# Kernel optimization log

Measured on AMD Instinct MI355X. Metric: run time of the kernel, lower is better.

Reference implementation:

```python
import jax, jax.numpy as jnp
import numpy as np

FEATURE_DIM = 2048
CROP_PE_DIM = 96
FULL = FEATURE_DIM + CROP_PE_DIM  # 2144
H1 = 1024
H2 = 512
NEG_SLOPE = 0.01


def leaky(x):
    return jnp.where(x >= 0, x, NEG_SLOPE * x)


def setup_inputs() -> dict:
    key = jax.random.key(0)
    ks = jax.random.split(key, 8)
    B, T = 512, 32
    features = jax.random.normal(ks[0], (B, T, FULL), dtype=jnp.float32)

    def lin(k, fan_in, fan_out):
        kw, kb = jax.random.split(k)
        bound = 1.0 / np.sqrt(fan_in)
        W = jax.random.uniform(kw, (fan_in, fan_out), minval=-bound, maxval=bound, dtype=jnp.float32)
        b = jax.random.uniform(kb, (fan_out,), minval=-bound, maxval=bound, dtype=jnp.float32)
        return W, b

    We, be = lin(ks[1], 2 * FULL, H1)
    W1a, b1a = lin(ks[2], H1, H1)
    W1b, b1b = lin(ks[3], H1, H2)
    W2a, b2a = lin(ks[4], H2, H2)
    W2b, b2b = lin(ks[5], H2, H2)
    Wd, bd = lin(ks[6], H2, 3)
    return {
        "features": features,
        "We": We, "be": be,
        "W1a": W1a, "b1a": b1a, "W1b": W1b, "b1b": b1b,
        "W2a": W2a, "b2a": b2a, "W2b": W2b, "b2b": b2b,
        "Wd": Wd, "bd": bd,
    }


def reference(features, We, be, W1a, b1a, W1b, b1b, W2a, b2a, W2b, b2b, Wd, bd):
    B, T, D = features.shape
    # Vectorized version of the double Python loop: pair each token with token 0.
    anchor = jnp.broadcast_to(features[:, :1, :], (B, T, D))  # features[i][0]
    features_full = jnp.concatenate((features, anchor), axis=-1).reshape(B * T, 2 * D)
    e_f = features_full @ We + be
    h = leaky(leaky(e_f) @ W1a + b1a)
    h = h @ W1b + b1b  # block1 output
    h2 = leaky(leaky(h) @ W2a + b2a) @ W2b + b2b  # block2
    h = h + h2
    translations = leaky(h) @ Wd + bd  # (B*T, 3)
    bias = jnp.array([[0.0, 0.0, 1.0]], dtype=translations.dtype)
    return translations + bias
```

## Files before the change

kernel.cpp:

```cpp
#include <hip/hip_runtime.h>
#include <hip/hip_bf16.h>
#include <stdint.h>

typedef __attribute__((ext_vector_type(4))) float f32x4;
typedef __attribute__((ext_vector_type(8))) short bf16x8;

#define BK 64

__device__ inline void gload_lds16(const void* g, void* l) {
    __builtin_amdgcn_global_load_lds(
        (const __attribute__((address_space(1))) void*)g,
        (__attribute__((address_space(3))) void*)l, 16, 0, 0);
}

__device__ inline void wg_barrier() {
    asm volatile("s_barrier" ::: "memory");
}
#define SCHED0 __builtin_amdgcn_sched_barrier(0)

__device__ inline int xcd_swizzle(int orig, int nwg) {
    int q = nwg >> 3, r = nwg & 7;
    int xcd = orig & 7, idx = orig >> 3;
    int base = (xcd < r) ? xcd * (q + 1) : r * (q + 1) + (xcd - r) * q;
    return base + idx;
}

__device__ inline float b2f(short s) {
    union { float f; unsigned u; } x; x.u = ((unsigned)(unsigned short)s) << 16; return x.f;
}
__device__ inline short f2bs(float f) {
    __hip_bfloat16 h = __float2bfloat16(f);
    short s; __builtin_memcpy(&s, &h, 2); return s;
}

__global__ __launch_bounds__(256) void cvt_feat(const float* __restrict__ in,
                                                __hip_bfloat16* __restrict__ out) {
    int i = blockIdx.x * 256 + threadIdx.x;
    const int CH = 16384 * 272;
    if (i >= CH) return;
    int r = i / 272, c8 = (i % 272) * 8;
    __hip_bfloat16 tmp[8];
    if (c8 < 2144) {
        const float4* p = (const float4*)(in + (size_t)r * 2144 + c8);
        float4 x0 = p[0], x1 = p[1];
        tmp[0] = __float2bfloat16(x0.x); tmp[1] = __float2bfloat16(x0.y);
        tmp[2] = __float2bfloat16(x0.z); tmp[3] = __float2bfloat16(x0.w);
        tmp[4] = __float2bfloat16(x1.x); tmp[5] = __float2bfloat16(x1.y);
        tmp[6] = __float2bfloat16(x1.z); tmp[7] = __float2bfloat16(x1.w);
    } else {
        #pragma unroll
        for (int j = 0; j < 8; j++) tmp[j] = __float2bfloat16(0.f);
    }
    *(bf16x8*)&out[(size_t)r * 2176 + c8] = *(const bf16x8*)tmp;
}

__global__ __launch_bounds__(256) void cvt_wt_t(const float* __restrict__ W,
                                                __hip_bfloat16* __restrict__ WT,
                                                int K, int N, int KP) {
    __shared__ float tile[32][33];
    const int ntn = N >> 5;
    const int tk = blockIdx.x / ntn, tn = blockIdx.x - tk * ntn;
    const int k0 = tk * 32, n0 = tn * 32;
    const int c = threadIdx.x & 31, r8 = threadIdx.x >> 5;
    #pragma unroll
    for (int p = 0; p < 4; p++) {
        int k = k0 + r8 + p * 8;
        tile[r8 + p * 8][c] = (k < K) ? W[(size_t)k * N + n0 + c] : 0.f;
    }
    __syncthreads();
    #pragma unroll
    for (int p = 0; p < 4; p++) {
        int n = n0 + r8 + p * 8;
        WT[(size_t)n * KP + k0 + c] = __float2bfloat16(tile[c][r8 + p * 8]);
    }
}

template<int BN_, int RES_MODE, int OUTK>
__global__ __launch_bounds__(512, 2)
void gemm8ph(const __hip_bfloat16* __restrict__ A, int lda,
             const __hip_bfloat16* __restrict__ Bt,
             const float* __restrict__ bias,
             const __hip_bfloat16* __restrict__ resb,
             const float* __restrict__ resf,
             __hip_bfloat16* __restrict__ outb,
             __hip_bfloat16* __restrict__ outb2,
             float* __restrict__ outf,
             int M, int N, int K, int gx)
{
    constexpr int NF  = BN_ / 64;
    constexpr int REL = NF * 16;
    __shared__ __hip_bfloat16 lds[2][(256 + BN_) * BK];

    const int nwg  = gridDim.x;
    const int wgid = xcd_swizzle(blockIdx.x, nwg);
    const int by   = wgid / gx;
    const int bx   = wgid - by * gx;

    const int t    = threadIdx.x;
    const int lane = t & 63;
    const int wv   = t >> 6;
    const int wr   = wv >> 2;
    const int wc   = wv & 3;

    const int row0 = by * 256;
    const int col0 = bx * BN_;

    const int NT = K / BK;
    const int split = blockIdx.y;
    const int kb = (split * NT) / gridDim.y;
    const int ke = ((split + 1) * NT) / gridDim.y;
    float* outfs = outf;
    if (OUTK == 0 && gridDim.y > 1) outfs = outf + (size_t)split * M * N;

    const int srow = t >> 3;
    const int scol = ((t & 7) * 8) ^ ((srow & 7) << 3);
    const int sdst = (t & 7) * 8;

    f32x4 acc[8][NF];
    #pragma unroll
    for (int i = 0; i < 8; i++)
        #pragma unroll
        for (int j = 0; j < NF; j++)
            acc[i][j] = f32x4{0.f, 0.f, 0.f, 0.f};

    const int lrow = lane & 15;
    const int lk   = (lane >> 4) * 8;
    const int rxor = (lrow & 7) << 3;

    auto stA = [&](int buf, int k0, int b) {
        gload_lds16(A + (size_t)(row0 + b * 64 + srow) * lda + k0 + scol,
                    &lds[buf][(b * 64 + srow) * BK + sdst]);
    };
    auto stB = [&](int buf, int k0, int b) {
        gload_lds16(Bt + (size_t)(col0 + b * 64 + srow) * K + k0 + scol,
                    &lds[buf][(256 + b * 64 + srow) * BK + sdst]);
    };
    auto rdA = [&](bf16x8 (&af)[4][2], int buf, int ih) {
        #pragma unroll
        for (int i = 0; i < 4; ++i)
            #pragma unroll
            for (int h = 0; h < 2; ++h)
                af[i][h] = *(const bf16x8*)
                    &lds[buf][(wr * 128 + (ih * 4 + i) * 16 + lrow) * BK + ((h * 32 + lk) ^ rxor)];
    };
    auto rdB = [&](bf16x8 (&bg)[2][2], int buf, int jb) {
        #pragma unroll
        for (int j = 0; j < 2; ++j)
            #pragma unroll
            for (int h = 0; h < 2; ++h)
                bg[j][h] = *(const bf16x8*)
                    &lds[buf][(256 + wc * REL + (jb + j) * 16 + lrow) * BK + ((h * 32 + lk) ^ rxor)];
    };

#define MFMA_Q(IB, JB)                                                        \
    do {                                                                      \
        __builtin_amdgcn_s_setprio(1);                                        \
        _Pragma("unroll") for (int h_ = 0; h_ < 2; ++h_)                      \
        _Pragma("unroll") for (int i_ = 0; i_ < 4; ++i_)                      \
        _Pragma("unroll") for (int j_ = 0; j_ < 2; ++j_)                      \
            acc[(IB) + i_][(JB) + j_] = __builtin_amdgcn_mfma_f32_16x16x32_bf16( \
                af[i_][h_], bg[j_][h_], acc[(IB) + i_][(JB) + j_], 0, 0, 0);  \
        __builtin_amdgcn_s_setprio(0);                                        \
    } while (0)

    {
        const int k0 = kb * BK;
        if constexpr (NF == 4) {
            stA(0, k0, 0); stA(0, k0, 2);
            stB(0, k0, 0); stB(0, k0, 1);
            stB(0, k0, 2); stB(0, k0, 3);
            stA(0, k0, 1); stA(0, k0, 3);
        } else {
            stA(0, k0, 0); stA(0, k0, 2);
            stB(0, k0, 0); stB(0, k0, 1);
            stA(0, k0, 1); stA(0, k0, 3);
        }
    }
    asm volatile("s_waitcnt vmcnt(2)" ::: "memory");
    wg_barrier();

    int cur = 0;
    for (int kt = kb; kt < ke; ++kt) {
        const bool pf = (kt + 1 < ke);
        const int nk0 = (kt + 1) * BK;
        bf16x8 af[4][2], bg[2][2];
        if constexpr (NF == 4) {
            rdA(af, cur, 0); rdB(bg, cur, 0);
            if (pf) { stA(cur ^ 1, nk0, 0); stA(cur ^ 1, nk0, 2); }
            wg_barrier(); SCHED0;
            MFMA_Q(0, 0);
            wg_barrier();
            rdB(bg, cur, 2);
            if (pf) { stB(cur ^ 1, nk0, 0); stB(cur ^ 1, nk0, 1); }
            if (pf) asm volatile("s_waitcnt vmcnt(4)" ::: "memory");
            else    asm volatile("s_waitcnt vmcnt(0)" ::: "memory");
            wg_barrier(); SCHED0;
            MFMA_Q(0, 2);
            wg_barrier();
            rdA(af, cur, 1); rdB(bg, cur, 0);
            if (pf) { stB(cur ^ 1, nk0, 2); stB(cur ^ 1, nk0, 3); }
            wg_barrier(); SCHED0;
            MFMA_Q(4, 0);
            wg_barrier();
            rdB(bg, cur, 2);
            if (pf) {
                stA(cur ^ 1, nk0, 1); stA(cur ^ 1, nk0, 3);
                asm volatile("s_waitcnt vmcnt(2)" ::: "memory");
            }
            wg_barrier(); SCHED0;
            MFMA_Q(4, 2);
            wg_barrier();
        } else {
            rdA(af, cur, 0); rdB(bg, cur, 0);
            if (pf) { stA(cur ^ 1, nk0, 0); stA(cur ^ 1, nk0, 2);
                      stB(cur ^ 1, nk0, 0); stB(cur ^ 1, nk0, 1); }
            if (pf) asm volatile("s_waitcnt vmcnt(4)" ::: "memory");
            else    asm volatile("s_waitcnt vmcnt(0)" ::: "memory");
            wg_barrier(); SCHED0;
            MFMA_Q(0, 0);
            wg_barrier();
            rdA(af, cur, 1);
            if (pf) {
                stA(cur ^ 1, nk0, 1); stA(cur ^ 1, nk0, 3);
                asm volatile("s_waitcnt vmcnt(2)" ::: "memory");
            }
            wg_barrier(); SCHED0;
            MFMA_Q(4, 0);
            wg_barrier();
        }
        cur ^= 1;
    }
#undef MFMA_Q

    if constexpr (OUTK == 0) {
        #pragma unroll
        for (int j = 0; j < NF; j++) {
            const int col = col0 + wc * REL + j * 16 + lrow;
            #pragma unroll
            for (int i = 0; i < 8; i++) {
                const int rbase = row0 + wr * 128 + i * 16 + (lane >> 4) * 4;
                #pragma unroll
                for (int r = 0; r < 4; r++)
                    outfs[(size_t)(rbase + r) * N + col] = acc[i][j][r];
            }
        }
    } else {
        wg_barrier();
        __hip_bfloat16* eb = &lds[0][0] + wv * (128 * REL);
        #pragma unroll
        for (int i = 0; i < 8; i++)
            #pragma unroll
            for (int j = 0; j < NF; j++)
                #pragma unroll
                for (int r = 0; r < 4; r++)
                    eb[(i * 16 + (lane >> 4) * 4 + r) * REL + j * 16 + lrow] =
                        __float2bfloat16(acc[i][j][r]);
        constexpr int LPR = REL / 8;
        constexpr int RPI = 64 / LPR;
        constexpr int NIT = 128 / RPI;
        const int lrr = lane / LPR;
        const int lcc = (lane % LPR) * 8;
        const int col = col0 + wc * REL + lcc;
        float bvv[8];
        if (bias) {
            float4 b0 = *(const float4*)&bias[col];
            float4 b1 = *(const float4*)&bias[col + 4];
            bvv[0] = b0.x; bvv[1] = b0.y; bvv[2] = b0.z; bvv[3] = b0.w;
            bvv[4] = b1.x; bvv[5] = b1.y; bvv[6] = b1.z; bvv[7] = b1.w;
        } else {
            #pragma unroll
            for (int e = 0; e < 8; e++) bvv[e] = 0.f;
        }
        #pragma unroll
        for (int it = 0; it < NIT; it++) {
            const int rl  = it * RPI + lrr;
            const int row = row0 + wr * 128 + rl;
            bf16x8 v8 = *(bf16x8*)&eb[rl * REL + lcc];
            float vv[8];
            #pragma unroll
            for (int e = 0; e < 8; e++) vv[e] = b2f(v8[e]) + bvv[e];
            if constexpr (RES_MODE == 1) {
                bf16x8 r8 = *(const bf16x8*)&resb[(size_t)row * N + col];
                #pragma unroll
                for (int e = 0; e < 8; e++) vv[e] += b2f(r8[e]);
            }
            if constexpr (RES_MODE == 2) {
                const float* rp = &resf[(size_t)(row >> 5) * N + col];
                float4 r0 = *(const float4*)rp;
                float4 r1 = *(const float4*)(rp + 4);
                vv[0] += r0.x; vv[1] += r0.y; vv[2] += r0.z; vv[3] += r0.w;
                vv[4] += r1.x; vv[5] += r1.y; vv[6] += r1.z; vv[7] += r1.w;
            }
            bf16x8 o1, o2;
            #pragma unroll
            for (int e = 0; e < 8; e++) {
                float lv = vv[e] >= 0.f ? vv[e] : 0.01f * vv[e];
                if constexpr (OUTK == 1) o1[e] = f2bs(lv);
                if constexpr (OUTK == 2) o1[e] = f2bs(vv[e]);
                if constexpr (OUTK == 3) { o1[e] = f2bs(lv); o2[e] = f2bs(vv[e]); }
            }
            *(bf16x8*)&outb[(size_t)row * N + col] = o1;
            if constexpr (OUTK == 3)
                *(bf16x8*)&outb2[(size_t)row * N + col] = o2;
        }
    }
}

__global__ __launch_bounds__(256)
void anchor_reduce(const float* __restrict__ part, const float* __restrict__ be,
                   float* __restrict__ out) {
    int i = blockIdx.x * 256 + threadIdx.x;
    if (i >= 512 * 1024) return;
    const int S = 512 * 1024;
    int col = i & 1023;
    float s = be[col];
    #pragma unroll
    for (int p = 0; p < 8; p++) s += part[i + p * S];
    out[i] = s;
}

__global__ __launch_bounds__(256)
void final_head(const __hip_bfloat16* __restrict__ h, const float* __restrict__ Wd,
                const float* __restrict__ bd, float* __restrict__ out)
{
    int row  = blockIdx.x * 4 + (threadIdx.x >> 6);
    int lane = threadIdx.x & 63;
    const __hip_bfloat16* hr = h + (size_t)row * 512;
    bf16x8 v8 = *(const bf16x8*)&hr[lane * 8];
    float s0 = 0.f, s1 = 0.f, s2 = 0.f;
    #pragma unroll
    for (int e = 0; e < 8; e++) {
        float v = b2f(v8[e]);
        v = v >= 0.f ? v : 0.01f * v;
        int k = lane * 8 + e;
        s0 += v * Wd[k * 3 + 0];
        s1 += v * Wd[k * 3 + 1];
        s2 += v * Wd[k * 3 + 2];
    }
    #pragma unroll
    for (int off = 32; off > 0; off >>= 1) {
        s0 += __shfl_down(s0, off);
        s1 += __shfl_down(s1, off);
        s2 += __shfl_down(s2, off);
    }
    if (lane == 0) {
        out[row * 3 + 0] = s0 + bd[0];
        out[row * 3 + 1] = s1 + bd[1];
        out[row * 3 + 2] = s2 + bd[2] + 1.0f;
    }
}

extern "C" void kernel_launch(void* const* d_in, const int* in_sizes, int n_in,
                              void* d_out, int out_size, void* d_ws, size_t ws_size,
                              hipStream_t stream)
{
    const float* features = (const float*)d_in[0];
    const float* We  = (const float*)d_in[1];
    const float* be  = (const float*)d_in[2];
    const float* W1a = (const float*)d_in[3];
    const float* b1a = (const float*)d_in[4];
    const float* W1b = (const float*)d_in[5];
    const float* b1b = (const float*)d_in[6];
    const float* W2a = (const float*)d_in[7];
    const float* b2a = (const float*)d_in[8];
    const float* W2b = (const float*)d_in[9];
    const float* b2b = (const float*)d_in[10];
    const float* Wd  = (const float*)d_in[11];
    const float* bd  = (const float*)d_in[12];
    float* out = (float*)d_out;

    char* ws = (char*)d_ws;
    size_t off = 0;
    auto alloc = [&](size_t bytes) -> char* {
        char* p = ws + off;
        off += (bytes + 255) & ~(size_t)255;
        return p;
    };
    __hip_bfloat16* featbf = (__hip_bfloat16*)alloc(16384ull * 2176 * 2);
    __hip_bfloat16* WeTt   = (__hip_bfloat16*)alloc(1024ull * 2176 * 2);
    __hip_bfloat16* WeTb   = (__hip_bfloat16*)alloc(1024ull * 2176 * 2);
    __hip_bfloat16* W1aT   = (__hip_bfloat16*)alloc(1024ull * 1024 * 2);
    __hip_bfloat16* W1bT   = (__hip_bfloat16*)alloc(512ull * 1024 * 2);
    __hip_bfloat16* W2aT   = (__hip_bfloat16*)alloc(512ull * 512 * 2);
    __hip_bfloat16* W2bT   = (__hip_bfloat16*)alloc(512ull * 512 * 2);
    float* eanchor_part    = (float*)alloc(8ull * 512 * 1024 * 4);
    float* eanchor         = (float*)alloc(512ull * 1024 * 4);
    char* bufA             = alloc(16384ull * 1024 * 2);
    char* bufB             = alloc(16384ull * 1024 * 2);
    __hip_bfloat16* h1b    = (__hip_bfloat16*)alloc(16384ull * 512 * 2);

    __hip_bfloat16* act1   = (__hip_bfloat16*)bufA;
    __hip_bfloat16* act2   = (__hip_bfloat16*)bufB;
    __hip_bfloat16* act3   = (__hip_bfloat16*)bufA;
    __hip_bfloat16* act4   = (__hip_bfloat16*)bufB;
    __hip_bfloat16* hsum_b = (__hip_bfloat16*)bufA;

    cvt_feat<<<(16384 * 272 + 255) / 256, 256, 0, stream>>>(features, featbf);
    cvt_wt_t<<<68 * 32, 256, 0, stream>>>(We,               WeTt, 2144, 1024, 2176);
    cvt_wt_t<<<68 * 32, 256, 0, stream>>>(We + 2144 * 1024, WeTb, 2144, 1024, 2176);
    cvt_wt_t<<<32 * 32, 256, 0, stream>>>(W1a, W1aT, 1024, 1024, 1024);
    cvt_wt_t<<<32 * 16, 256, 0, stream>>>(W1b, W1bT, 1024, 512, 1024);
    cvt_wt_t<<<16 * 16, 256, 0, stream>>>(W2a, W2aT, 512, 512, 512);
    cvt_wt_t<<<16 * 16, 256, 0, stream>>>(W2b, W2bT, 512, 512, 512);

    gemm8ph<256, 0, 0><<<dim3(8, 8), 512, 0, stream>>>(
        featbf, 32 * 2176, WeTb, nullptr, nullptr, nullptr,
        nullptr, nullptr, eanchor_part, 512, 1024, 2176, 4);
    anchor_reduce<<<2048, 256, 0, stream>>>(eanchor_part, be, eanchor);

    gemm8ph<256, 2, 1><<<dim3(256), 512, 0, stream>>>(
        featbf, 2176, WeTt, nullptr, nullptr, eanchor,
        act1, nullptr, nullptr, 16384, 1024, 2176, 4);

    gemm8ph<256, 0, 1><<<dim3(256), 512, 0, stream>>>(
        act1, 1024, W1aT, b1a, nullptr, nullptr,
        act2, nullptr, nullptr, 16384, 1024, 1024, 4);

    gemm8ph<128, 0, 3><<<dim3(256), 512, 0, stream>>>(
        act2, 1024, W1bT, b1b, nullptr, nullptr,
        act3, h1b, nullptr, 16384, 512, 1024, 4);

    gemm8ph<128, 0, 1><<<dim3(256), 512, 0, stream>>>(
        act3, 512, W2aT, b2a, nullptr, nullptr,
        act4, nullptr, nullptr, 16384, 512, 512, 4);

    gemm8ph<128, 1, 2><<<dim3(256), 512, 0, stream>>>(
        act4, 512, W2bT, b2b, h1b, nullptr,
        hsum_b, nullptr, nullptr, 16384, 512, 512, 4);

    final_head<<<4096, 256, 0, stream>>>(hsum_b, Wd, bd, out);
}
```

Baseline: 257.0 us.

## Fuse fp32-to-bf16 feature conversion into first GEMM's A-tile loads

Removes the separate cvt_feat kernel and its bf16 feature buffer. The encoder GEMMs now read fp32 features directly into registers, convert them to bf16, and write them into swizzled LDS, zero-padding the K tail. The main loop is also restructured to load all B fragments once per k-step and to issue A/B loads in consolidated groups with new waitcnt placement. This saves a full pass writing and re-reading 16384x2176 bf16, at the cost of doubling global A traffic (fp32) inside the GEMM and extra register pressure for the staging registers and B fragments.

```diff
diff --git a/kernel.cpp b/kernel.cpp
--- a/kernel.cpp
+++ b/kernel.cpp
@@ -31,27 +31,6 @@
 __device__ inline short f2bs(float f) {
     __hip_bfloat16 h = __float2bfloat16(f);
     short s; __builtin_memcpy(&s, &h, 2); return s;
-}
-
-__global__ __launch_bounds__(256) void cvt_feat(const float* __restrict__ in,
-                                                __hip_bfloat16* __restrict__ out) {
-    int i = blockIdx.x * 256 + threadIdx.x;
-    const int CH = 16384 * 272;
-    if (i >= CH) return;
-    int r = i / 272, c8 = (i % 272) * 8;
-    __hip_bfloat16 tmp[8];
-    if (c8 < 2144) {
-        const float4* p = (const float4*)(in + (size_t)r * 2144 + c8);
-        float4 x0 = p[0], x1 = p[1];
-        tmp[0] = __float2bfloat16(x0.x); tmp[1] = __float2bfloat16(x0.y);
-        tmp[2] = __float2bfloat16(x0.z); tmp[3] = __float2bfloat16(x0.w);
-        tmp[4] = __float2bfloat16(x1.x); tmp[5] = __float2bfloat16(x1.y);
-        tmp[6] = __float2bfloat16(x1.z); tmp[7] = __float2bfloat16(x1.w);
-    } else {
-        #pragma unroll
-        for (int j = 0; j < 8; j++) tmp[j] = __float2bfloat16(0.f);
-    }
-    *(bf16x8*)&out[(size_t)r * 2176 + c8] = *(const bf16x8*)tmp;
 }
 
 __global__ __launch_bounds__(256) void cvt_wt_t(const float* __restrict__ W,
@@ -75,21 +54,24 @@
     }
 }
 
-template<int BN_, int RES_MODE, int OUTK>
+template<int BN_, int RES_MODE, int OUTK, bool AF32>
 __global__ __launch_bounds__(512, 2)
-void gemm8ph(const __hip_bfloat16* __restrict__ A, int lda,
-             const __hip_bfloat16* __restrict__ Bt,
-             const float* __restrict__ bias,
-             const __hip_bfloat16* __restrict__ resb,
-             const float* __restrict__ resf,
-             __hip_bfloat16* __restrict__ outb,
-             __hip_bfloat16* __restrict__ outb2,
-             float* __restrict__ outf,
-             int M, int N, int K, int gx)
+void gemmk(const void* __restrict__ Asrc, int lda, int amult, int Kreal,
+           const __hip_bfloat16* __restrict__ Bt,
+           const float* __restrict__ bias,
+           const __hip_bfloat16* __restrict__ resb,
+           const float* __restrict__ resf,
+           __hip_bfloat16* __restrict__ outb,
+           __hip_bfloat16* __restrict__ outb2,
+           float* __restrict__ outf,
+           int M, int N, int K, int gx)
 {
     constexpr int NF  = BN_ / 64;
     constexpr int REL = NF * 16;
     __shared__ __hip_bfloat16 lds[2][(256 + BN_) * BK];
+
+    const float*          Af = (const float*)Asrc;
+    const __hip_bfloat16* Ab = (const __hip_bfloat16*)Asrc;
 
     const int nwg  = gridDim.x;
     const int wgid = xcd_swizzle(blockIdx.x, nwg);
@@ -113,8 +95,10 @@
     if (OUTK == 0 && gridDim.y > 1) outfs = outf + (size_t)split * M * N;
 
     const int srow = t >> 3;
-    const int scol = ((t & 7) * 8) ^ ((srow & 7) << 3);
-    const int sdst = (t & 7) * 8;
+    const int sc8  = (t & 7) * 8;
+    const int sswz = (srow & 7) << 3;
+    const int scol = sc8 ^ sswz;
+    const int sdst = sc8;
 
     f32x4 acc[8][NF];
     #pragma unroll
@@ -127,29 +111,58 @@
     const int lk   = (lane >> 4) * 8;
     const int rxor = (lrow & 7) << 3;
 
-    auto stA = [&](int buf, int k0, int b) {
-        gload_lds16(A + (size_t)(row0 + b * 64 + srow) * lda + k0 + scol,
-                    &lds[buf][(b * 64 + srow) * BK + sdst]);
-    };
-    auto stB = [&](int buf, int k0, int b) {
-        gload_lds16(Bt + (size_t)(col0 + b * 64 + srow) * K + k0 + scol,
-                    &lds[buf][(256 + b * 64 + srow) * BK + sdst]);
-    };
-    auto rdA = [&](bf16x8 (&af)[4][2], int buf, int ih) {
+    float4 sreg[8] = {};
+
+    auto stA_all = [&](int buf, int k0) {
+        #pragma unroll
+        for (int b = 0; b < 4; ++b)
+            gload_lds16(Ab + (size_t)(row0 + b * 64 + srow) * lda + k0 + scol,
+                        &lds[buf][(b * 64 + srow) * BK + sdst]);
+    };
+    auto ldA_all = [&](int k0) {
+        const int gc = k0 + sc8;
+        const bool v = gc < Kreal;
+        #pragma unroll
+        for (int b = 0; b < 4; ++b) {
+            const float* p = Af + (size_t)(row0 + b * 64 + srow) * (size_t)amult * lda + gc;
+            sreg[b * 2 + 0] = v ? *(const float4*)p       : float4{0.f, 0.f, 0.f, 0.f};
+            sreg[b * 2 + 1] = v ? *(const float4*)(p + 4) : float4{0.f, 0.f, 0.f, 0.f};
+        }
+    };
+    auto wrA_all = [&](int buf) {
+        #pragma unroll
+        for (int b = 0; b < 4; ++b) {
+            float4 x0 = sreg[b * 2], x1 = sreg[b * 2 + 1];
+            bf16x8 w;
+            w[0] = f2bs(x0.x); w[1] = f2bs(x0.y); w[2] = f2bs(x0.z); w[3] = f2bs(x0.w);
+            w[4] = f2bs(x1.x); w[5] = f2bs(x1.y); w[6] = f2bs(x1.z); w[7] = f2bs(x1.w);
+            *(bf16x8*)&lds[buf][(b * 64 + srow) * BK + (sc8 ^ sswz)] = w;
+        }
+    };
+    auto stB_all = [&](int buf, int k0) {
+        #pragma unroll
+        for (int b = 0; b < NF; ++b)
+            gload_lds16(Bt + (size_t)(col0 + b * 64 + srow) * K + k0 + scol,
+                        &lds[buf][(256 + b * 64 + srow) * BK + sdst]);
+    };
+
+    bf16x8 bgall[NF][2];
+    auto rdB_all = [&](int buf) {
+        #pragma unroll
+        for (int j = 0; j < NF; ++j)
+            #pragma unroll
+            for (int h = 0; h < 2; ++h)
+                bgall[j][h] = *(const bf16x8*)
+                    &lds[buf][(256 + wc * REL + j * 16 + lrow) * BK + ((h * 32 + lk) ^ rxor)];
+    };
+    bf16x8 af[4][2];
+    auto rdA = [&](int buf, int ih) {
         #pragma unroll
         for (int i = 0; i < 4; ++i)
             #pragma unroll
             for (int h = 0; h < 2; ++h)
                 af[i][h] = *(const bf16x8*)
                     &lds[buf][(wr * 128 + (ih * 4 + i) * 16 + lrow) * BK + ((h * 32 + lk) ^ rxor)];
-    };
-    auto rdB = [&](bf16x8 (&bg)[2][2], int buf, int jb) {
-        #pragma unroll
-        for (int j = 0; j < 2; ++j)
-            #pragma unroll
-            for (int h = 0; h < 2; ++h)
-                bg[j][h] = *(const bf16x8*)
-                    &lds[buf][(256 + wc * REL + (jb + j) * 16 + lrow) * BK + ((h * 32 + lk) ^ rxor)];
     };
 
 #define MFMA_Q(IB, JB)                                                        \
@@ -159,73 +172,75 @@
         _Pragma("unroll") for (int i_ = 0; i_ < 4; ++i_)                      \
         _Pragma("unroll") for (int j_ = 0; j_ < 2; ++j_)                      \
             acc[(IB) + i_][(JB) + j_] = __builtin_amdgcn_mfma_f32_16x16x32_bf16( \
-                af[i_][h_], bg[j_][h_], acc[(IB) + i_][(JB) + j_], 0, 0, 0);  \
+                af[i_][h_], bgall[(JB) + j_][h_], acc[(IB) + i_][(JB) + j_], 0, 0, 0); \
         __builtin_amdgcn_s_setprio(0);                                        \
     } while (0)
 
     {
         const int k0 = kb * BK;
-        if constexpr (NF == 4) {
-            stA(0, k0, 0); stA(0, k0, 2);
-            stB(0, k0, 0); stB(0, k0, 1);
-            stB(0, k0, 2); stB(0, k0, 3);
-            stA(0, k0, 1); stA(0, k0, 3);
+        if constexpr (AF32) {
+            ldA_all(k0);
+            stB_all(0, k0);
+            if constexpr (NF == 4) asm volatile("s_waitcnt vmcnt(4)" ::: "memory");
+            else                   asm volatile("s_waitcnt vmcnt(2)" ::: "memory");
+            wrA_all(0);
+            asm volatile("s_waitcnt vmcnt(0) lgkmcnt(0)" ::: "memory");
         } else {
-            stA(0, k0, 0); stA(0, k0, 2);
-            stB(0, k0, 0); stB(0, k0, 1);
-            stA(0, k0, 1); stA(0, k0, 3);
-        }
-    }
-    asm volatile("s_waitcnt vmcnt(2)" ::: "memory");
-    wg_barrier();
+            stA_all(0, k0);
+            stB_all(0, k0);
+            asm volatile("s_waitcnt vmcnt(0)" ::: "memory");
+        }
+        wg_barrier();
+    }
 
     int cur = 0;
     for (int kt = kb; kt < ke; ++kt) {
         const bool pf = (kt + 1 < ke);
         const int nk0 = (kt + 1) * BK;
-        bf16x8 af[4][2], bg[2][2];
         if constexpr (NF == 4) {
-            rdA(af, cur, 0); rdB(bg, cur, 0);
-            if (pf) { stA(cur ^ 1, nk0, 0); stA(cur ^ 1, nk0, 2); }
+            rdB_all(cur); rdA(cur, 0);
+            if (pf) { if constexpr (AF32) ldA_all(nk0); else stA_all(cur ^ 1, nk0); }
             wg_barrier(); SCHED0;
             MFMA_Q(0, 0);
             wg_barrier();
-            rdB(bg, cur, 2);
-            if (pf) { stB(cur ^ 1, nk0, 0); stB(cur ^ 1, nk0, 1); }
-            if (pf) asm volatile("s_waitcnt vmcnt(4)" ::: "memory");
-            else    asm volatile("s_waitcnt vmcnt(0)" ::: "memory");
+            if (pf) stB_all(cur ^ 1, nk0);
             wg_barrier(); SCHED0;
             MFMA_Q(0, 2);
             wg_barrier();
-            rdA(af, cur, 1); rdB(bg, cur, 0);
-            if (pf) { stB(cur ^ 1, nk0, 2); stB(cur ^ 1, nk0, 3); }
+            rdA(cur, 1);
+            if constexpr (AF32) {
+                if (pf) {
+                    asm volatile("s_waitcnt vmcnt(4)" ::: "memory");
+                    wrA_all(cur ^ 1);
+                }
+            }
             wg_barrier(); SCHED0;
             MFMA_Q(4, 0);
             wg_barrier();
-            rdB(bg, cur, 2);
+            MFMA_Q(4, 2);
+            if constexpr (AF32) asm volatile("s_waitcnt vmcnt(0) lgkmcnt(0)" ::: "memory");
+            else                asm volatile("s_waitcnt vmcnt(0)" ::: "memory");
+            wg_barrier();
+        } else {
+            rdB_all(cur); rdA(cur, 0);
             if (pf) {
-                stA(cur ^ 1, nk0, 1); stA(cur ^ 1, nk0, 3);
-                asm volatile("s_waitcnt vmcnt(2)" ::: "memory");
-            }
-            wg_barrier(); SCHED0;
-            MFMA_Q(4, 2);
-            wg_barrier();
-        } else {
-            rdA(af, cur, 0); rdB(bg, cur, 0);
-            if (pf) { stA(cur ^ 1, nk0, 0); stA(cur ^ 1, nk0, 2);
-                      stB(cur ^ 1, nk0, 0); stB(cur ^ 1, nk0, 1); }
-            if (pf) asm volatile("s_waitcnt vmcnt(4)" ::: "memory");
-            else    asm volatile("s_waitcnt vmcnt(0)" ::: "memory");
+                if constexpr (AF32) ldA_all(nk0); else stA_all(cur ^ 1, nk0);
+                stB_all(cur ^ 1, nk0);
+            }
             wg_barrier(); SCHED0;
             MFMA_Q(0, 0);
             wg_barrier();
-            rdA(af, cur, 1);
-            if (pf) {
-                stA(cur ^ 1, nk0, 1); stA(cur ^ 1, nk0, 3);
-                asm volatile("s_waitcnt vmcnt(2)" ::: "memory");
+            rdA(cur, 1);
+            if constexpr (AF32) {
+                if (pf) {
+                    asm volatile("s_waitcnt vmcnt(2)" ::: "memory");
+                    wrA_all(cur ^ 1);
+                }
             }
             wg_barrier(); SCHED0;
             MFMA_Q(4, 0);
+            if constexpr (AF32) asm volatile("s_waitcnt vmcnt(0) lgkmcnt(0)" ::: "memory");
+            else                asm volatile("s_waitcnt vmcnt(0)" ::: "memory");
             wg_barrier();
         }
         cur ^= 1;
@@ -376,7 +391,6 @@
         off += (bytes + 255) & ~(size_t)255;
         return p;
     };
-    __hip_bfloat16* featbf = (__hip_bfloat16*)alloc(16384ull * 2176 * 2);
     __hip_bfloat16* WeTt   = (__hip_bfloat16*)alloc(1024ull * 2176 * 2);
     __hip_bfloat16* WeTb   = (__hip_bfloat16*)alloc(1024ull * 2176 * 2);
     __hip_bfloat16* W1aT   = (__hip_bfloat16*)alloc(1024ull * 1024 * 2);
@@ -395,7 +409,6 @@
     __hip_bfloat16* act4   = (__hip_bfloat16*)bufB;
     __hip_bfloat16* hsum_b = (__hip_bfloat16*)bufA;
 
-    cvt_feat<<<(16384 * 272 + 255) / 256, 256, 0, stream>>>(features, featbf);
     cvt_wt_t<<<68 * 32, 256, 0, stream>>>(We,               WeTt, 2144, 1024, 2176);
     cvt_wt_t<<<68 * 32, 256, 0, stream>>>(We + 2144 * 1024, WeTb, 2144, 1024, 2176);
     cvt_wt_t<<<32 * 32, 256, 0, stream>>>(W1a, W1aT, 1024, 1024, 1024);
@@ -403,29 +416,29 @@
     cvt_wt_t<<<16 * 16, 256, 0, stream>>>(W2a, W2aT, 512, 512, 512);
     cvt_wt_t<<<16 * 16, 256, 0, stream>>>(W2b, W2bT, 512, 512, 512);
 
-    gemm8ph<256, 0, 0><<<dim3(8, 8), 512, 0, stream>>>(
-        featbf, 32 * 2176, WeTb, nullptr, nullptr, nullptr,
+    gemmk<256, 0, 0, true><<<dim3(8, 8), 512, 0, stream>>>(
+        features, 2144, 32, 2144, WeTb, nullptr, nullptr, nullptr,
         nullptr, nullptr, eanchor_part, 512, 1024, 2176, 4);
     anchor_reduce<<<2048, 256, 0, stream>>>(eanchor_part, be, eanchor);
 
-    gemm8ph<256, 2, 1><<<dim3(256), 512, 0, stream>>>(
-        featbf, 2176, WeTt, nullptr, nullptr, eanchor,
+    gemmk<256, 2, 1, true><<<dim3(256), 512, 0, stream>>>(
+        features, 2144, 1, 2144, WeTt, nullptr, nullptr, eanchor,
         act1, nullptr, nullptr, 16384, 1024, 2176, 4);
 
-    gemm8ph<256, 0, 1><<<dim3(256), 512, 0, stream>>>(
-        act1, 1024, W1aT, b1a, nullptr, nullptr,
+    gemmk<256, 0, 1, false><<<dim3(256), 512, 0, stream>>>(
+        act1, 1024, 1, 1024, W1aT, b1a, nullptr, nullptr,
         act2, nullptr, nullptr, 16384, 1024, 1024, 4);
 
-    gemm8ph<128, 0, 3><<<dim3(256), 512, 0, stream>>>(
-        act2, 1024, W1bT, b1b, nullptr, nullptr,
+    gemmk<128, 0, 3, false><<<dim3(256), 512, 0, stream>>>(
+        act2, 1024, 1, 1024, W1bT, b1b, nullptr, nullptr,
         act3, h1b, nullptr, 16384, 512, 1024, 4);
 
-    gemm8ph<128, 0, 1><<<dim3(256), 512, 0, stream>>>(
-        act3, 512, W2aT, b2a, nullptr, nullptr,
+    gemmk<128, 0, 1, false><<<dim3(256), 512, 0, stream>>>(
+        act3, 512, 1, 512, W2aT, b2a, nullptr, nullptr,
         act4, nullptr, nullptr, 16384, 512, 512, 4);
 
-    gemm8ph<128, 1, 2><<<dim3(256), 512, 0, stream>>>(
-        act4, 512, W2bT, b2b, h1b, nullptr,
+    gemmk<128, 1, 2, false><<<dim3(256), 512, 0, stream>>>(
+        act4, 512, 1, 512, W2bT, b2b, h1b, nullptr,
         hsum_b, nullptr, nullptr, 16384, 512, 512, 4);
 
     final_head<<<4096, 256, 0, stream>>>(hsum_b, Wd, bd, out);
```

After: 271.6 us. +5.7%, slower.

## Restructure GEMM main loop: load all B fragments once, bulk prefetch stages

Applied to the files above, without the earlier changes.

Reworks the GEMM k-loop schedule. All B fragments are read from LDS once per k-tile into registers, replacing repeated per-quarter reads. Global-to-LDS prefetches are issued in larger groups, with a single full vmcnt(0) wait at the end of each iteration instead of staggered partial waits. This cuts LDS read traffic and one barrier phase, but raises register pressure and reduces how finely memory latency overlaps with MFMA work.

```diff
diff --git a/kernel.cpp b/kernel.cpp
--- a/kernel.cpp
+++ b/kernel.cpp
@@ -77,15 +77,15 @@
 
 template<int BN_, int RES_MODE, int OUTK>
 __global__ __launch_bounds__(512, 2)
-void gemm8ph(const __hip_bfloat16* __restrict__ A, int lda,
-             const __hip_bfloat16* __restrict__ Bt,
-             const float* __restrict__ bias,
-             const __hip_bfloat16* __restrict__ resb,
-             const float* __restrict__ resf,
-             __hip_bfloat16* __restrict__ outb,
-             __hip_bfloat16* __restrict__ outb2,
-             float* __restrict__ outf,
-             int M, int N, int K, int gx)
+void gemmk(const __hip_bfloat16* __restrict__ A, int lda,
+           const __hip_bfloat16* __restrict__ Bt,
+           const float* __restrict__ bias,
+           const __hip_bfloat16* __restrict__ resb,
+           const float* __restrict__ resf,
+           __hip_bfloat16* __restrict__ outb,
+           __hip_bfloat16* __restrict__ outb2,
+           float* __restrict__ outf,
+           int M, int N, int K, int gx)
 {
     constexpr int NF  = BN_ / 64;
     constexpr int REL = NF * 16;
@@ -113,8 +113,9 @@
     if (OUTK == 0 && gridDim.y > 1) outfs = outf + (size_t)split * M * N;
 
     const int srow = t >> 3;
-    const int scol = ((t & 7) * 8) ^ ((srow & 7) << 3);
-    const int sdst = (t & 7) * 8;
+    const int sc8  = (t & 7) * 8;
+    const int scol = sc8 ^ ((srow & 7) << 3);
+    const int sdst = sc8;
 
     f32x4 acc[8][NF];
     #pragma unroll
@@ -127,29 +128,36 @@
     const int lk   = (lane >> 4) * 8;
     const int rxor = (lrow & 7) << 3;
 
-    auto stA = [&](int buf, int k0, int b) {
-        gload_lds16(A + (size_t)(row0 + b * 64 + srow) * lda + k0 + scol,
-                    &lds[buf][(b * 64 + srow) * BK + sdst]);
+    auto stA_all = [&](int buf, int k0) {
+        #pragma unroll
+        for (int b = 0; b < 4; ++b)
+            gload_lds16(A + (size_t)(row0 + b * 64 + srow) * lda + k0 + scol,
+                        &lds[buf][(b * 64 + srow) * BK + sdst]);
     };
-    auto stB = [&](int buf, int k0, int b) {
-        gload_lds16(Bt + (size_t)(col0 + b * 64 + srow) * K + k0 + scol,
-                    &lds[buf][(256 + b * 64 + srow) * BK + sdst]);
+    auto stB_all = [&](int buf, int k0) {
+        #pragma unroll
+        for (int b = 0; b < NF; ++b)
+            gload_lds16(Bt + (size_t)(col0 + b * 64 + srow) * K + k0 + scol,
+                        &lds[buf][(256 + b * 64 + srow) * BK + sdst]);
     };
-    auto rdA = [&](bf16x8 (&af)[4][2], int buf, int ih) {
+
+    bf16x8 bgall[NF][2];
+    auto rdB_all = [&](int buf) {
+        #pragma unroll
+        for (int j = 0; j < NF; ++j)
+            #pragma unroll
+            for (int h = 0; h < 2; ++h)
+                bgall[j][h] = *(const bf16x8*)
+                    &lds[buf][(256 + wc * REL + j * 16 + lrow) * BK + ((h * 32 + lk) ^ rxor)];
+    };
+    bf16x8 af[4][2];
+    auto rdA = [&](int buf, int ih) {
         #pragma unroll
         for (int i = 0; i < 4; ++i)
             #pragma unroll
             for (int h = 0; h < 2; ++h)
                 af[i][h] = *(const bf16x8*)
                     &lds[buf][(wr * 128 + (ih * 4 + i) * 16 + lrow) * BK + ((h * 32 + lk) ^ rxor)];
-    };
-    auto rdB = [&](bf16x8 (&bg)[2][2], int buf, int jb) {
-        #pragma unroll
-        for (int j = 0; j < 2; ++j)
-            #pragma unroll
-            for (int h = 0; h < 2; ++h)
-                bg[j][h] = *(const bf16x8*)
-                    &lds[buf][(256 + wc * REL + (jb + j) * 16 + lrow) * BK + ((h * 32 + lk) ^ rxor)];
     };
 
 #define MFMA_Q(IB, JB)                                                        \
@@ -159,73 +167,49 @@
         _Pragma("unroll") for (int i_ = 0; i_ < 4; ++i_)                      \
         _Pragma("unroll") for (int j_ = 0; j_ < 2; ++j_)                      \
             acc[(IB) + i_][(JB) + j_] = __builtin_amdgcn_mfma_f32_16x16x32_bf16( \
-                af[i_][h_], bg[j_][h_], acc[(IB) + i_][(JB) + j_], 0, 0, 0);  \
+                af[i_][h_], bgall[(JB) + j_][h_], acc[(IB) + i_][(JB) + j_], 0, 0, 0); \
         __builtin_amdgcn_s_setprio(0);                                        \
     } while (0)
 
     {
         const int k0 = kb * BK;
-        if constexpr (NF == 4) {
-            stA(0, k0, 0); stA(0, k0, 2);
-            stB(0, k0, 0); stB(0, k0, 1);
-            stB(0, k0, 2); stB(0, k0, 3);
-            stA(0, k0, 1); stA(0, k0, 3);
-        } else {
-            stA(0, k0, 0); stA(0, k0, 2);
-            stB(0, k0, 0); stB(0, k0, 1);
-            stA(0, k0, 1); stA(0, k0, 3);
-        }
-    }
-    asm volatile("s_waitcnt vmcnt(2)" ::: "memory");
-    wg_barrier();
+        stA_all(0, k0);
+        stB_all(0, k0);
+        asm volatile("s_waitcnt vmcnt(0)" ::: "memory");
+        wg_barrier();
+    }
 
     int cur = 0;
     for (int kt = kb; kt < ke; ++kt) {
         const bool pf = (kt + 1 < ke);
         const int nk0 = (kt + 1) * BK;
-        bf16x8 af[4][2], bg[2][2];
         if constexpr (NF == 4) {
-            rdA(af, cur, 0); rdB(bg, cur, 0);
-            if (pf) { stA(cur ^ 1, nk0, 0); stA(cur ^ 1, nk0, 2); }
+            rdB_all(cur); rdA(cur, 0);
+            if (pf) stA_all(cur ^ 1, nk0);
             wg_barrier(); SCHED0;
             MFMA_Q(0, 0);
             wg_barrier();
-            rdB(bg, cur, 2);
-            if (pf) { stB(cur ^ 1, nk0, 0); stB(cur ^ 1, nk0, 1); }
-            if (pf) asm volatile("s_waitcnt vmcnt(4)" ::: "memory");
-            else    asm volatile("s_waitcnt vmcnt(0)" ::: "memory");
+            if (pf) stB_all(cur ^ 1, nk0);
             wg_barrier(); SCHED0;
             MFMA_Q(0, 2);
             wg_barrier();
-            rdA(af, cur, 1); rdB(bg, cur, 0);
-            if (pf) { stB(cur ^ 1, nk0, 2); stB(cur ^ 1, nk0, 3); }
+            rdA(cur, 1);
             wg_barrier(); SCHED0;
             MFMA_Q(4, 0);
             wg_barrier();
-            rdB(bg, cur, 2);
-            if (pf) {
-                stA(cur ^ 1, nk0, 1); stA(cur ^ 1, nk0, 3);
-                asm volatile("s_waitcnt vmcnt(2)" ::: "memory");
-            }
-            wg_barrier(); SCHED0;
             MFMA_Q(4, 2);
+            asm volatile("s_waitcnt vmcnt(0)" ::: "memory");
             wg_barrier();
         } else {
-            rdA(af, cur, 0); rdB(bg, cur, 0);
-            if (pf) { stA(cur ^ 1, nk0, 0); stA(cur ^ 1, nk0, 2);
-                      stB(cur ^ 1, nk0, 0); stB(cur ^ 1, nk0, 1); }
-            if (pf) asm volatile("s_waitcnt vmcnt(4)" ::: "memory");
-            else    asm volatile("s_waitcnt vmcnt(0)" ::: "memory");
+            rdB_all(cur); rdA(cur, 0);
+            if (pf) { stA_all(cur ^ 1, nk0); stB_all(cur ^ 1, nk0); }
             wg_barrier(); SCHED0;
             MFMA_Q(0, 0);
             wg_barrier();
-            rdA(af, cur, 1);
-            if (pf) {
-                stA(cur ^ 1, nk0, 1); stA(cur ^ 1, nk0, 3);
-                asm volatile("s_waitcnt vmcnt(2)" ::: "memory");
-            }
+            rdA(cur, 1);
             wg_barrier(); SCHED0;
             MFMA_Q(4, 0);
+            asm volatile("s_waitcnt vmcnt(0)" ::: "memory");
             wg_barrier();
         }
         cur ^= 1;
@@ -403,28 +387,28 @@
     cvt_wt_t<<<16 * 16, 256, 0, stream>>>(W2a, W2aT, 512, 512, 512);
     cvt_wt_t<<<16 * 16, 256, 0, stream>>>(W2b, W2bT, 512, 512, 512);
 
-    gemm8ph<256, 0, 0><<<dim3(8, 8), 512, 0, stream>>>(
+    gemmk<256, 0, 0><<<dim3(8, 8), 512, 0, stream>>>(
         featbf, 32 * 2176, WeTb, nullptr, nullptr, nullptr,
         nullptr, nullptr, eanchor_part, 512, 1024, 2176, 4);
     anchor_reduce<<<2048, 256, 0, stream>>>(eanchor_part, be, eanchor);
 
-    gemm8ph<256, 2, 1><<<dim3(256), 512, 0, stream>>>(
+    gemmk<256, 2, 1><<<dim3(256), 512, 0, stream>>>(
         featbf, 2176, WeTt, nullptr, nullptr, eanchor,
         act1, nullptr, nullptr, 16384, 1024, 2176, 4);
 
-    gemm8ph<256, 0, 1><<<dim3(256), 512, 0, stream>>>(
+    gemmk<256, 0, 1><<<dim3(256), 512, 0, stream>>>(
         act1, 1024, W1aT, b1a, nullptr, nullptr,
         act2, nullptr, nullptr, 16384, 1024, 1024, 4);
 
-    gemm8ph<128, 0, 3><<<dim3(256), 512, 0, stream>>>(
+    gemmk<128, 0, 3><<<dim3(256), 512, 0, stream>>>(
         act2, 1024, W1bT, b1b, nullptr, nullptr,
         act3, h1b, nullptr, 16384, 512, 1024, 4);
 
-    gemm8ph<128, 0, 1><<<dim3(256), 512, 0, stream>>>(
+    gemmk<128, 0, 1><<<dim3(256), 512, 0, stream>>>(
         act3, 512, W2aT, b2a, nullptr, nullptr,
         act4, nullptr, nullptr, 16384, 512, 512, 4);
 
-    gemm8ph<128, 1, 2><<<dim3(256), 512, 0, stream>>>(
+    gemmk<128, 1, 2><<<dim3(256), 512, 0, stream>>>(
         act4, 512, W2bT, b2b, h1b, nullptr,
         hsum_b, nullptr, nullptr, 16384, 512, 512, 4);
 
```

After: 253.9 us. About the same (-1.2%).
